# Kernel tuning notes

Measured on AMD Instinct MI355X. Metric: run time of the kernel, lower is better.

## Reference

```python
import jax, jax.numpy as jnp
import numpy as np
from jax import lax

B, CIN, COUT, K, H, W = 16, 512, 512, 3, 64, 64
STYLE_DIM, BASIS, DIRS = 512, 8, 8


def setup_inputs() -> dict:
    key = jax.random.key(0)
    ks = jax.random.split(key, 8)
    return {
        "x": jax.random.normal(ks[0], (B, CIN, H, W), jnp.float32),
        "style": jax.random.normal(ks[1], (B, STYLE_DIM), jnp.float32),
        "weight": jax.random.normal(ks[2], (1, COUT, CIN, K, K), jnp.float32),
        "mod_w": jax.random.normal(ks[3], (CIN, STYLE_DIM), jnp.float32) * 0.02,
        "mod_b": jnp.ones((CIN,), jnp.float32),
        "basis_vectors": jax.random.normal(ks[4], (BASIS, 1, COUT, CIN, K, K), jnp.float32),
        "shifts_coords": jax.random.normal(ks[5], (DIRS, BASIS), jnp.float32),
        "batch_shifts": jax.random.uniform(ks[6], (B,), jnp.float32),
        "batch_directions": jax.random.randint(ks[7], (B,), 0, DIRS),
    }


def reference(x, style, weight, mod_w, mod_b, basis_vectors, shifts_coords,
              batch_shifts, batch_directions):
    batch, in_ch, h, w = x.shape
    out_ch, k = weight.shape[1], weight.shape[3]
    scale = 1.0 / np.sqrt(in_ch * k * k)  # StyleGAN2 equalized-lr scale

    # --- deformation: per-sample weight delta from basis subspace ---
    coefs = shifts_coords[batch_directions]                     # [B, basis]
    bv = basis_vectors.reshape(basis_vectors.shape[0], -1)      # [basis, O*I*k*k]
    delta = coefs @ bv                                          # [B, P]
    nrm = jnp.linalg.norm(delta, axis=1, keepdims=True)
    delta = delta / jnp.maximum(nrm, 1e-12) * batch_shifts[:, None]
    delta = delta.reshape(batch, out_ch, in_ch, k, k)
    wgt = weight + delta                                        # [B, O, I, k, k]

    # --- style modulation + demodulation ---
    s = style @ mod_w.T + mod_b                                 # [B, I]
    wgt = scale * wgt * s[:, None, :, None, None]
    demod = lax.rsqrt(jnp.sum(wgt * wgt, axis=(2, 3, 4)) + 1e-8)  # [B, O]
    wgt = wgt * demod[:, :, None, None, None]

    # --- grouped conv, groups = batch ---
    wgt = wgt.reshape(batch * out_ch, in_ch, k, k)
    xg = x.reshape(1, batch * in_ch, h, w)
    pad = k // 2
    out = lax.conv_general_dilated(
        xg, wgt, window_strides=(1, 1), padding=[(pad, pad), (pad, pad)],
        feature_group_count=batch,
        dimension_numbers=("NCHW", "OIHW", "NCHW"))
    return out.reshape(batch, out_ch, h, w)
```

## Files before the change

kernel.cpp:

```cpp
#include <hip/hip_runtime.h>


typedef __attribute__((ext_vector_type(8))) short bf16x8;
typedef __attribute__((ext_vector_type(4))) float f32x4;
typedef float f32x4u __attribute__((ext_vector_type(4), aligned(4)));

__device__ __forceinline__ unsigned short f2bf(float f) {
  unsigned u = __float_as_uint(f);
  return (unsigned short)((u + 0x7FFFu + ((u >> 16) & 1u)) >> 16);
}

__device__ __forceinline__ void gl_lds16(const void* g, void* l) {
  __builtin_amdgcn_global_load_lds(
      (const __attribute__((address_space(1))) void*)g,
      (__attribute__((address_space(3))) void*)l, 16, 0, 0);
}

template <int N> __device__ __forceinline__ void vm_wait() {
  if constexpr (N == 8) asm volatile("s_waitcnt vmcnt(8)" ::: "memory");
  else if constexpr (N == 0) asm volatile("s_waitcnt vmcnt(0)" ::: "memory");
}

__global__ __launch_bounds__(256) void k_pad(const float* __restrict__ x,
                                             unsigned short* __restrict__ xp) {
  const int bx = blockIdx.x;
  const int b   = bx >> 9;
  const int rem = bx & 511;
  const int y   = rem >> 3;
  const int cb  = rem & 7;
  const int t = threadIdx.x;
  __shared__ float tile[64][65];
  const float* src = x + ((size_t)(b * 512 + cb * 64) * 4096) + y * 64;
#pragma unroll
  for (int r = 0; r < 4; ++r) {
    int idx = r * 256 + t;
    int ch = idx >> 4;
    int xq = (idx & 15) << 2;
    float4 v = *(const float4*)(src + (size_t)ch * 4096 + xq);
    tile[ch][xq + 0] = v.x; tile[ch][xq + 1] = v.y;
    tile[ch][xq + 2] = v.z; tile[ch][xq + 3] = v.w;
  }
  const uint4 z4 = {0u, 0u, 0u, 0u};
  if (t < 16) {
    const int side = t >> 3;
    const int lo = (t & 7) * 8;
    unsigned short* p =
        xp + (((size_t)(b * 66 + y + 1) * 66 + side * 65) * 512 + cb * 64 + lo);
    *(uint4*)p = z4;
  }
  if (y == 0 || y == 63) {
    const int row = (y == 0) ? 0 : 65;
    for (int idx = t; idx < 528; idx += 256) {
      const int c = idx >> 3;
      const int lo = (idx & 7) * 8;
      unsigned short* p =
          xp + (((size_t)(b * 66 + row) * 66 + c) * 512 + cb * 64 + lo);
      *(uint4*)p = z4;
    }
  }
  __syncthreads();
  const int col = t >> 2;
  const int q = t & 3;
  union { unsigned short u16[16]; uint4 v[2]; } pk;
#pragma unroll
  for (int j = 0; j < 16; ++j) pk.u16[j] = f2bf(tile[q * 16 + j][col]);
  unsigned short* dst =
      xp + (((size_t)(b * 66 + y + 1) * 66 + col + 1) * 512 + cb * 64 + q * 16);
  *(uint4*)dst = pk.v[0];
  *(uint4*)(dst + 8) = pk.v[1];
}

__global__ __launch_bounds__(256) void k_mod(const float* __restrict__ style,
                                             const float* __restrict__ mod_w,
                                             const float* __restrict__ mod_b,
                                             float* __restrict__ smod) {
  const int b = blockIdx.x;
  __shared__ float st[512];
  for (int d = threadIdx.x; d < 512; d += 256) st[d] = style[b * 512 + d];
  __syncthreads();
  for (int i = threadIdx.x; i < 512; i += 256) {
    const float* wr = mod_w + (size_t)i * 512;
    float acc = 0.f;
#pragma unroll 4
    for (int d = 0; d < 512; d += 4) {
      float4 wv = *(const float4*)(wr + d);
      acc += wv.x * st[d] + wv.y * st[d + 1] + wv.z * st[d + 2] + wv.w * st[d + 3];
    }
    smod[b * 512 + i] = acc + mod_b[i];
  }
}

__global__ __launch_bounds__(256, 3) void k_gram(const float* __restrict__ bv,
                                                 float* __restrict__ G) {
  const int P4 = 589824;
  float a[36];
#pragma unroll
  for (int c = 0; c < 36; ++c) a[c] = 0.f;
  const float4* bv4 = (const float4*)bv;
  for (int p = blockIdx.x * 256 + threadIdx.x; p < P4; p += gridDim.x * 256) {
    float4 v[8];
#pragma unroll
    for (int k = 0; k < 8; ++k) v[k] = bv4[(size_t)k * P4 + p];
    int c = 0;
#pragma unroll
    for (int i = 0; i < 8; ++i)
#pragma unroll
      for (int j = i; j < 8; ++j) {
        a[c] += v[i].x * v[j].x + v[i].y * v[j].y + v[i].z * v[j].z +
                v[i].w * v[j].w;
        ++c;
      }
  }
#pragma unroll
  for (int c = 0; c < 36; ++c)
#pragma unroll
    for (int off = 32; off > 0; off >>= 1) a[c] += __shfl_down(a[c], off);
  __shared__ float red[4][36];
  const int wv = threadIdx.x >> 6;
  if ((threadIdx.x & 63) == 0)
#pragma unroll
    for (int c = 0; c < 36; ++c) red[wv][c] = a[c];
  __syncthreads();
  if (threadIdx.x < 36)
    atomicAdd(&G[threadIdx.x], red[0][threadIdx.x] + red[1][threadIdx.x] +
                                   red[2][threadIdx.x] + red[3][threadIdx.x]);
}

__global__ __launch_bounds__(512, 2) void k_weights(
    const float* __restrict__ weight, const float* __restrict__ bv,
    const float* __restrict__ smod, const float* __restrict__ G,
    const float* __restrict__ shifts_coords,
    const float* __restrict__ batch_shifts, const int* __restrict__ dirs,
    unsigned short* __restrict__ wgt, float* __restrict__ demod) {
  const int o = blockIdx.x;
  const int i = threadIdx.x;
  __shared__ float cl[128];
  __shared__ float red[8][16];
  if (threadIdx.x < 16) {
    const int b = threadIdx.x;
    const int dir = dirs[b];
    float c[8];
#pragma unroll
    for (int k = 0; k < 8; ++k) c[k] = shifts_coords[dir * 8 + k];
    float n2 = 0.f;
    int idx = 0;
#pragma unroll
    for (int ii = 0; ii < 8; ++ii)
#pragma unroll
      for (int j = ii; j < 8; ++j) {
        float g = G[idx++];
        n2 += (ii == j) ? c[ii] * c[ii] * g : 2.f * c[ii] * c[j] * g;
      }
    const float amp =
        batch_shifts[b] / fmaxf(sqrtf(fmaxf(n2, 0.f)), 1e-12f);
#pragma unroll
    for (int k = 0; k < 8; ++k) cl[b * 8 + k] = c[k] * amp;
  }
  __syncthreads();
  const float scl = 0.014731391274719738f;
  const size_t base = ((size_t)o * 512 + i) * 9;
  float w9[9], v9[8][9];
  {
    f32x4u a = *(const f32x4u*)(weight + base);
    f32x4u c = *(const f32x4u*)(weight + base + 4);
    w9[0] = a.x; w9[1] = a.y; w9[2] = a.z; w9[3] = a.w;
    w9[4] = c.x; w9[5] = c.y; w9[6] = c.z; w9[7] = c.w;
    w9[8] = weight[base + 8];
  }
#pragma unroll
  for (int k = 0; k < 8; ++k) {
    const float* pk_ = bv + (size_t)k * 2359296 + base;
    f32x4u a = *(const f32x4u*)(pk_);
    f32x4u c = *(const f32x4u*)(pk_ + 4);
    v9[k][0] = a.x; v9[k][1] = a.y; v9[k][2] = a.z; v9[k][3] = a.w;
    v9[k][4] = c.x; v9[k][5] = c.y; v9[k][6] = c.z; v9[k][7] = c.w;
    v9[k][8] = pk_[8];
  }
  float ssq[16];
#pragma unroll
  for (int b = 0; b < 16; ++b) ssq[b] = 0.f;
#pragma unroll
  for (int b = 0; b < 16; ++b) {
    const float sm_b = smod[b * 512 + i] * scl;
#pragma unroll
    for (int kk = 0; kk < 9; ++kk) {
      float d = w9[kk];
#pragma unroll
      for (int k = 0; k < 8; ++k) d = fmaf(cl[b * 8 + k], v9[k][kk], d);
      const float wv = d * sm_b;
      ssq[b] = fmaf(wv, wv, ssq[b]);
      wgt[(((size_t)(b * 9 + kk) * 512 + o) << 9) + i] = f2bf(wv);
    }
  }
#pragma unroll
  for (int b = 0; b < 16; ++b)
#pragma unroll
    for (int off = 32; off > 0; off >>= 1) ssq[b] += __shfl_down(ssq[b], off);
  const int wv_ = threadIdx.x >> 6;
  if ((threadIdx.x & 63) == 0)
#pragma unroll
    for (int b = 0; b < 16; ++b) red[wv_][b] = ssq[b];
  __syncthreads();
  if (threadIdx.x < 16) {
    float s = 0.f;
#pragma unroll
    for (int wq = 0; wq < 8; ++wq) s += red[wq][threadIdx.x];
    demod[threadIdx.x * 512 + o] = rsqrtf(s + 1e-8f);
  }
}

__global__ __launch_bounds__(512, 2) void k_conv(
    const unsigned short* __restrict__ xp, const unsigned short* __restrict__ wgt,
    const float* __restrict__ demod, float* __restrict__ out) {
  extern __shared__ unsigned char smem[];
  const int tid = threadIdx.x;
  const int l = tid & 63;
  const int w = tid >> 6;
  const int wo = w >> 2;
  const int wn = w & 3;

  const int bid = blockIdx.x;
  const int bz = (bid & 7) * 64 + (bid >> 3);
  const int b = bz >> 5;
  const int tt = bz & 31;
  const int o0 = (tt >> 4) << 8;
  const int tn = tt & 15;
  const int n0 = tn << 8;
  const int y0 = tn << 2;

  int swzS[4];
  size_t aByte[4], pBase[4];
#pragma unroll
  for (int r = 0; r < 4; ++r) {
    const int idx = r * 512 + tid;
    const int row = idx >> 3;
    const int swz = ((idx & 7) << 4) ^ ((row & 7) << 4);
    swzS[r] = swz;
    aByte[r] = ((size_t)(o0 + row) << 10) + swz;
    pBase[r] = (size_t)(b * 66 + y0 + (row >> 6)) * 66 + (row & 63);
  }

  const char* wgtc = (const char*)wgt;
  const char* xpc = (const char*)xp;

  auto stage_all = [&](unsigned char* buf, int kt) {
    const int kk = kt >> 3;
    const int is = kt & 7;
    const int ky = kk / 3;
    const int kx = kk - ky * 3;
    const size_t aPlane = ((size_t)(b * 9 + kk) << 19) + ((size_t)is << 7);
    unsigned char* lA = buf;
    unsigned char* lB = buf + 32768;
#pragma unroll
    for (int r = 0; r < 4; ++r)
      gl_lds16(wgtc + aPlane + aByte[r], lA + (r * 512 + tid) * 16);
#pragma unroll
    for (int r = 0; r < 4; ++r)
      gl_lds16(xpc + (((pBase[r] + ky * 66 + kx) << 10) + ((size_t)is << 7) +
                      swzS[r]),
               lB + (r * 512 + tid) * 16);
  };

  f32x4 acc[8][4];
  const f32x4 zz = {0.f, 0.f, 0.f, 0.f};
#pragma unroll
  for (int mi = 0; mi < 8; ++mi)
#pragma unroll
    for (int ni = 0; ni < 4; ++ni) acc[mi][ni] = zz;
  bf16x8 af0[8], af1[8], bf0[4], bf1[4];

  auto rdA = [&](const unsigned char* lA, int MH, bf16x8 (&afx)[8]) {
#pragma unroll
    for (int mi = 0; mi < 4; ++mi)
#pragma unroll
      for (int ks = 0; ks < 2; ++ks) {
        const int row = MH * 128 + wo * 64 + mi * 16 + (l & 15);
        afx[mi * 2 + ks] = *(const bf16x8*)(
            lA + row * 128 + ((ks * 64 + ((l >> 4) << 4)) ^ ((row & 7) << 4)));
      }
  };
  auto rdB = [&](const unsigned char* lB, int NH, bf16x8 (&bfx)[4]) {
#pragma unroll
    for (int ni = 0; ni < 2; ++ni)
#pragma unroll
      for (int ks = 0; ks < 2; ++ks) {
        const int row = NH * 128 + wn * 32 + ni * 16 + (l & 15);
        bfx[ni * 2 + ks] = *(const bf16x8*)(
            lB + row * 128 + ((ks * 64 + ((l >> 4) << 4)) ^ ((row & 7) << 4)));
      }
  };
  auto mma = [&](int MH, int NH, bf16x8 (&afx)[8], bf16x8 (&bfx)[4]) {
    __builtin_amdgcn_s_setprio(1);
#pragma unroll
    for (int mi = 0; mi < 4; ++mi)
#pragma unroll
      for (int ni = 0; ni < 2; ++ni)
#pragma unroll
        for (int ks = 0; ks < 2; ++ks)
          acc[MH * 4 + mi][NH * 2 + ni] =
              __builtin_amdgcn_mfma_f32_16x16x32_bf16(
                  afx[mi * 2 + ks], bfx[ni * 2 + ks],
                  acc[MH * 4 + mi][NH * 2 + ni], 0, 0, 0);
    __builtin_amdgcn_s_setprio(0);
  };

  stage_all(smem, 0);
  stage_all(smem + 65536, 1);
  vm_wait<8>();
  __builtin_amdgcn_s_barrier();

  int cur = 0;
#pragma unroll 1
  for (int kt = 0; kt < 72; ++kt) {
    unsigned char* lA = smem + (cur << 16);
    unsigned char* lB = lA + 32768;
    rdA(lA, 0, af0);
    rdB(lB, 0, bf0);
    rdB(lB, 1, bf1);
    rdA(lA, 1, af1);
    mma(0, 0, af0, bf0);
    mma(0, 1, af0, bf1);
    asm volatile("s_waitcnt lgkmcnt(0)" ::: "memory");
    __builtin_amdgcn_sched_barrier(0);
    __builtin_amdgcn_s_barrier();
    __builtin_amdgcn_sched_barrier(0);
    if (kt < 70) stage_all(lA, kt + 2);
    mma(1, 1, af1, bf1);
    mma(1, 0, af1, bf0);
    if (kt < 70) {
      vm_wait<8>();
      __builtin_amdgcn_s_barrier();
      __builtin_amdgcn_sched_barrier(0);
    } else if (kt == 70) {
      vm_wait<0>();
      __builtin_amdgcn_s_barrier();
      __builtin_amdgcn_sched_barrier(0);
    }
    cur ^= 1;
  }

  float* outb = out + (size_t)(b * 512 + o0) * 4096 + n0;
#pragma unroll
  for (int mh = 0; mh < 2; ++mh)
#pragma unroll
    for (int mi = 0; mi < 4; ++mi) {
      const int orow = mh * 128 + wo * 64 + mi * 16 + ((l >> 4) << 2);
      float dm[4];
#pragma unroll
      for (int r = 0; r < 4; ++r) dm[r] = demod[b * 512 + o0 + orow + r];
#pragma unroll
      for (int nh = 0; nh < 2; ++nh)
#pragma unroll
        for (int ni = 0; ni < 2; ++ni) {
          const int pix = nh * 128 + wn * 32 + ni * 16 + (l & 15);
#pragma unroll
          for (int r = 0; r < 4; ++r)
            outb[(size_t)(orow + r) * 4096 + pix] =
                acc[mh * 4 + mi][nh * 2 + ni][r] * dm[r];
        }
    }
}

extern "C" void kernel_launch(void* const* d_in, const int* in_sizes, int n_in,
                              void* d_out, int out_size, void* d_ws,
                              size_t ws_size, hipStream_t stream) {
  const float* x      = (const float*)d_in[0];
  const float* style  = (const float*)d_in[1];
  const float* weight = (const float*)d_in[2];
  const float* mod_w  = (const float*)d_in[3];
  const float* mod_b  = (const float*)d_in[4];
  const float* bv     = (const float*)d_in[5];
  const float* sc     = (const float*)d_in[6];
  const float* bsh    = (const float*)d_in[7];
  const int*   bdir   = (const int*)d_in[8];
  float* out = (float*)d_out;

  char* ws = (char*)d_ws;
  unsigned short* xp  = (unsigned short*)(ws);
  unsigned short* wgt = (unsigned short*)(ws + 71368704);
  float* G     = (float*)(ws + 146866176);
  float* smod  = (float*)(ws + 146866944);
  float* demod = (float*)(ws + 146899712);

  hipFuncSetAttribute((const void*)k_conv,
                      hipFuncAttributeMaxDynamicSharedMemorySize, 131072);

  hipMemsetAsync(G, 0, 256, stream);
  k_pad<<<8192, 256, 0, stream>>>(x, xp);
  k_mod<<<16, 256, 0, stream>>>(style, mod_w, mod_b, smod);
  k_gram<<<1024, 256, 0, stream>>>(bv, G);
  k_weights<<<512, 512, 0, stream>>>(weight, bv, smod, G, sc, bsh, bdir, wgt,
                                     demod);
  k_conv<<<512, 512, 131072, stream>>>(xp, wgt, demod, out);
}
```

Measured before the change: 416.0 us.

## Halve conv K-step, triple-buffer A tiles and shrink LDS footprint

The conv main loop moves from 72 K-steps of 64 channels to 144 steps of 32 channels. The A (weight) tile becomes triple-buffered and B stays double-buffered, so the next A stage can be issued right after the mid-loop barrier without waiting for the whole previous buffer to drain. The LDS swizzle is redone for 64-byte rows, and dynamic LDS drops from 128KB to 80KB. Smaller stages mean less data in flight per step, but also twice as many barriers and more loop overhead.

After: 429.3 us. 3.2% more time.

```diff
diff --git a/kernel.cpp b/kernel.cpp
--- a/kernel.cpp
+++ b/kernel.cpp
@@ -17,7 +17,7 @@
 }
 
 template <int N> __device__ __forceinline__ void vm_wait() {
-  if constexpr (N == 8) asm volatile("s_waitcnt vmcnt(8)" ::: "memory");
+  if constexpr (N == 4) asm volatile("s_waitcnt vmcnt(4)" ::: "memory");
   else if constexpr (N == 0) asm volatile("s_waitcnt vmcnt(0)" ::: "memory");
 }
 
@@ -218,6 +218,8 @@
   const int w = tid >> 6;
   const int wo = w >> 2;
   const int wn = w & 3;
+  const int lq = l & 15;
+  const int ls = l >> 4;
 
   const int bid = blockIdx.x;
   const int bz = (bid & 7) * 64 + (bid >> 3);
@@ -228,37 +230,40 @@
   const int n0 = tn << 8;
   const int y0 = tn << 2;
 
-  int swzS[4];
-  size_t aByte[4], pBase[4];
-#pragma unroll
-  for (int r = 0; r < 4; ++r) {
+  unsigned aOff[2];
+#pragma unroll
+  for (int r = 0; r < 2; ++r) {
     const int idx = r * 512 + tid;
-    const int row = idx >> 3;
-    const int swz = ((idx & 7) << 4) ^ ((row & 7) << 4);
-    swzS[r] = swz;
-    aByte[r] = ((size_t)(o0 + row) << 10) + swz;
-    pBase[r] = (size_t)(b * 66 + y0 + (row >> 6)) * 66 + (row & 63);
+    const int row = idx >> 2;
+    const int sl = (idx & 3) ^ ((row >> 1) & 3);
+    aOff[r] = ((unsigned)(o0 + row) << 10) + sl * 16;
+  }
+  size_t pB[2];
+#pragma unroll
+  for (int r = 0; r < 2; ++r) {
+    const int idx = r * 512 + tid;
+    const int row = idx >> 2;
+    const int sl = (idx & 3) ^ ((row >> 1) & 3);
+    pB[r] = ((size_t)((b * 66 + y0 + (row >> 6)) * 66 + (row & 63)) << 10) +
+            sl * 16;
   }
 
   const char* wgtc = (const char*)wgt;
   const char* xpc = (const char*)xp;
 
-  auto stage_all = [&](unsigned char* buf, int kt) {
-    const int kk = kt >> 3;
-    const int is = kt & 7;
+  auto stage = [&](unsigned char* bufA, unsigned char* bufB, int s) {
+    const int kk = s >> 4;
+    const int is = s & 15;
     const int ky = kk / 3;
     const int kx = kk - ky * 3;
-    const size_t aPlane = ((size_t)(b * 9 + kk) << 19) + ((size_t)is << 7);
-    unsigned char* lA = buf;
-    unsigned char* lB = buf + 32768;
-#pragma unroll
-    for (int r = 0; r < 4; ++r)
-      gl_lds16(wgtc + aPlane + aByte[r], lA + (r * 512 + tid) * 16);
-#pragma unroll
-    for (int r = 0; r < 4; ++r)
-      gl_lds16(xpc + (((pBase[r] + ky * 66 + kx) << 10) + ((size_t)is << 7) +
-                      swzS[r]),
-               lB + (r * 512 + tid) * 16);
+    const size_t aPl = ((size_t)(b * 9 + kk) << 19) + ((unsigned)is << 6);
+    const unsigned bPl = ((unsigned)(ky * 66 + kx) << 10) + ((unsigned)is << 6);
+#pragma unroll
+    for (int r = 0; r < 2; ++r)
+      gl_lds16(wgtc + aPl + aOff[r], bufA + (r * 512 + tid) * 16);
+#pragma unroll
+    for (int r = 0; r < 2; ++r)
+      gl_lds16(xpc + pB[r] + bPl, bufB + (r * 512 + tid) * 16);
   };
 
   f32x4 acc[8][4];
@@ -267,76 +272,70 @@
   for (int mi = 0; mi < 8; ++mi)
 #pragma unroll
     for (int ni = 0; ni < 4; ++ni) acc[mi][ni] = zz;
-  bf16x8 af0[8], af1[8], bf0[4], bf1[4];
-
-  auto rdA = [&](const unsigned char* lA, int MH, bf16x8 (&afx)[8]) {
+  bf16x8 af0[4], af1[4], bf0[2], bf1[2];
+
+  auto rdA = [&](const unsigned char* lA, int MH, bf16x8 (&a4)[4]) {
+#pragma unroll
+    for (int mi = 0; mi < 4; ++mi) {
+      const int row = MH * 128 + wo * 64 + mi * 16 + lq;
+      a4[mi] = *(const bf16x8*)(lA + row * 64 + ((ls ^ ((row >> 1) & 3)) << 4));
+    }
+  };
+  auto rdB = [&](const unsigned char* lB, int NH, bf16x8 (&b2)[2]) {
+#pragma unroll
+    for (int ni = 0; ni < 2; ++ni) {
+      const int row = wn * 64 + NH * 32 + ni * 16 + lq;
+      b2[ni] = *(const bf16x8*)(lB + row * 64 + ((ls ^ ((row >> 1) & 3)) << 4));
+    }
+  };
+  auto mma8 = [&](int MH, int NH, bf16x8 (&a4)[4], bf16x8 (&b2)[2]) {
+    __builtin_amdgcn_s_setprio(1);
 #pragma unroll
     for (int mi = 0; mi < 4; ++mi)
 #pragma unroll
-      for (int ks = 0; ks < 2; ++ks) {
-        const int row = MH * 128 + wo * 64 + mi * 16 + (l & 15);
-        afx[mi * 2 + ks] = *(const bf16x8*)(
-            lA + row * 128 + ((ks * 64 + ((l >> 4) << 4)) ^ ((row & 7) << 4)));
-      }
-  };
-  auto rdB = [&](const unsigned char* lB, int NH, bf16x8 (&bfx)[4]) {
-#pragma unroll
-    for (int ni = 0; ni < 2; ++ni)
-#pragma unroll
-      for (int ks = 0; ks < 2; ++ks) {
-        const int row = NH * 128 + wn * 32 + ni * 16 + (l & 15);
-        bfx[ni * 2 + ks] = *(const bf16x8*)(
-            lB + row * 128 + ((ks * 64 + ((l >> 4) << 4)) ^ ((row & 7) << 4)));
-      }
-  };
-  auto mma = [&](int MH, int NH, bf16x8 (&afx)[8], bf16x8 (&bfx)[4]) {
-    __builtin_amdgcn_s_setprio(1);
-#pragma unroll
-    for (int mi = 0; mi < 4; ++mi)
-#pragma unroll
       for (int ni = 0; ni < 2; ++ni)
-#pragma unroll
-        for (int ks = 0; ks < 2; ++ks)
-          acc[MH * 4 + mi][NH * 2 + ni] =
-              __builtin_amdgcn_mfma_f32_16x16x32_bf16(
-                  afx[mi * 2 + ks], bfx[ni * 2 + ks],
-                  acc[MH * 4 + mi][NH * 2 + ni], 0, 0, 0);
+        acc[MH * 4 + mi][NH * 2 + ni] =
+            __builtin_amdgcn_mfma_f32_16x16x32_bf16(
+                a4[mi], b2[ni], acc[MH * 4 + mi][NH * 2 + ni], 0, 0, 0);
     __builtin_amdgcn_s_setprio(0);
   };
 
-  stage_all(smem, 0);
-  stage_all(smem + 65536, 1);
-  vm_wait<8>();
+  unsigned char* A0 = smem;
+  unsigned char* A1 = smem + 16384;
+  unsigned char* A2 = smem + 32768;
+  unsigned char* B0 = smem + 49152;
+  unsigned char* B1 = smem + 65536;
+
+  stage(A0, B0, 0);
+  stage(A1, B1, 1);
+  vm_wait<4>();
   __builtin_amdgcn_s_barrier();
-
-  int cur = 0;
+  __builtin_amdgcn_sched_barrier(0);
+
 #pragma unroll 1
-  for (int kt = 0; kt < 72; ++kt) {
-    unsigned char* lA = smem + (cur << 16);
-    unsigned char* lB = lA + 32768;
-    rdA(lA, 0, af0);
+  for (int t = 0; t < 144; ++t) {
+    const unsigned char* lB = (t & 1) ? B1 : B0;
+    unsigned char* sB = (t & 1) ? B1 : B0;
+    rdA(A0, 0, af0);
     rdB(lB, 0, bf0);
     rdB(lB, 1, bf1);
-    rdA(lA, 1, af1);
-    mma(0, 0, af0, bf0);
-    mma(0, 1, af0, bf1);
-    asm volatile("s_waitcnt lgkmcnt(0)" ::: "memory");
+    mma8(0, 0, af0, bf0);
+    mma8(0, 1, af0, bf1);
     __builtin_amdgcn_sched_barrier(0);
     __builtin_amdgcn_s_barrier();
     __builtin_amdgcn_sched_barrier(0);
-    if (kt < 70) stage_all(lA, kt + 2);
-    mma(1, 1, af1, bf1);
-    mma(1, 0, af1, bf0);
-    if (kt < 70) {
-      vm_wait<8>();
+    rdA(A0, 1, af1);
+    if (t < 142) stage(A2, sB, t + 2);
+    mma8(1, 1, af1, bf1);
+    mma8(1, 0, af1, bf0);
+    __builtin_amdgcn_sched_barrier(0);
+    if (t < 142) vm_wait<4>();
+    else if (t == 142) vm_wait<0>();
+    if (t < 143) {
       __builtin_amdgcn_s_barrier();
       __builtin_amdgcn_sched_barrier(0);
-    } else if (kt == 70) {
-      vm_wait<0>();
-      __builtin_amdgcn_s_barrier();
-      __builtin_amdgcn_sched_barrier(0);
-    }
-    cur ^= 1;
+    }
+    unsigned char* tmp = A0; A0 = A1; A1 = A2; A2 = tmp;
   }
 
   float* outb = out + (size_t)(b * 512 + o0) * 4096 + n0;
@@ -344,7 +343,7 @@
   for (int mh = 0; mh < 2; ++mh)
 #pragma unroll
     for (int mi = 0; mi < 4; ++mi) {
-      const int orow = mh * 128 + wo * 64 + mi * 16 + ((l >> 4) << 2);
+      const int orow = mh * 128 + wo * 64 + mi * 16 + ls * 4;
       float dm[4];
 #pragma unroll
       for (int r = 0; r < 4; ++r) dm[r] = demod[b * 512 + o0 + orow + r];
@@ -352,7 +351,7 @@
       for (int nh = 0; nh < 2; ++nh)
 #pragma unroll
         for (int ni = 0; ni < 2; ++ni) {
-          const int pix = nh * 128 + wn * 32 + ni * 16 + (l & 15);
+          const int pix = wn * 64 + nh * 32 + ni * 16 + lq;
 #pragma unroll
           for (int r = 0; r < 4; ++r)
             outb[(size_t)(orow + r) * 4096 + pix] =
@@ -382,14 +381,14 @@
   float* smod  = (float*)(ws + 146866944);
   float* demod = (float*)(ws + 146899712);
 
-  hipFuncSetAttribute((const void*)k_conv,
-                      hipFuncAttributeMaxDynamicSharedMemorySize, 131072);
-
-  hipMemsetAsync(G, 0, 256, stream);
+  (void)hipFuncSetAttribute((const void*)k_conv,
+                            hipFuncAttributeMaxDynamicSharedMemorySize, 81920);
+
+  (void)hipMemsetAsync(G, 0, 256, stream);
   k_pad<<<8192, 256, 0, stream>>>(x, xp);
   k_mod<<<16, 256, 0, stream>>>(style, mod_w, mod_b, smod);
   k_gram<<<1024, 256, 0, stream>>>(bv, G);
   k_weights<<<512, 512, 0, stream>>>(weight, bv, smod, G, sc, bsh, bdir, wgt,
                                      demod);
-  k_conv<<<512, 512, 131072, stream>>>(xp, wgt, demod, out);
-}
+  k_conv<<<512, 512, 81920, stream>>>(xp, wgt, demod, out);
+}
```
